# Performance work log

Measured on AMD Instinct MI355X. Metric: run time of the kernel, lower is better.

Reference implementation:

```python
import jax, jax.numpy as jnp
import numpy as np

B, L, E, V = 4, 2048, 1024, 64
NT = V * (V - 1) // 2  # 2016 upper-triangular entries
LN_EPS = 1e-5


def setup_inputs() -> dict:
    key = jax.random.key(0)
    ks = jax.random.split(key, 9)
    s = lambda d: 1.0 / np.sqrt(d)
    return {
        "hx": jax.random.normal(ks[0], (B, L, E), dtype=jnp.float32),
        "W_dense": jax.random.normal(ks[1], (E, E), dtype=jnp.float32) * s(E),
        "b_dense": jnp.zeros((E,), dtype=jnp.float32),
        "ln_g": jnp.ones((E,), dtype=jnp.float32),
        "ln_b": jnp.zeros((E,), dtype=jnp.float32),
        "W_theta": jax.random.normal(ks[2], (V, E), dtype=jnp.float32) * s(E),
        "b_theta": jnp.zeros((V,), dtype=jnp.float32),
        "W_Theta": jax.random.normal(ks[3], (NT, E), dtype=jnp.float32) * s(E),
        "b_Theta": jnp.zeros((NT,), dtype=jnp.float32),
    }


def reference(hx, W_dense, b_dense, ln_g, ln_b, W_theta, b_theta, W_Theta, b_Theta):
    # dense -> exact (erf) gelu -> LayerNorm (ESM1bLayerNorm)
    h = jax.nn.gelu(hx @ W_dense.T + b_dense, approximate=False)
    mu = jnp.mean(h, axis=-1, keepdims=True)
    var = jnp.mean(jnp.square(h - mu), axis=-1, keepdims=True)
    h = (h - mu) / jnp.sqrt(var + LN_EPS) * ln_g + ln_b

    pi = jax.nn.softmax(h @ W_theta.T + b_theta, axis=-1)          # (B,L,V)
    Theta = jax.nn.softplus(h @ W_Theta.T + b_Theta)               # (B,L,NT)

    iu, ju = np.triu_indices(V, k=1)
    S = jnp.zeros((B, L, V, V), dtype=h.dtype).at[:, :, iu, ju].set(Theta)
    S = S + jnp.swapaxes(S, -2, -1)                                # symmetric, zero diag

    # diag(1/sqrt(pi)) @ S @ diag(sqrt(pi)) == S * sqrt(pi_j)/sqrt(pi_i)
    pi_sqrt = jnp.sqrt(pi)
    Q = S * (pi_sqrt[..., None, :] / pi_sqrt[..., :, None])
    Q = Q - Q.sum(axis=-1)[..., :, None] * jnp.eye(V, dtype=Q.dtype)
    return (Q, pi)
```

## Files before the change

### kernel.cpp

```cpp
#include <hip/hip_runtime.h>
#include <hip/hip_bf16.h>
#include <cstdint>
#include <cstddef>

#define MROWS 8192
#define EDIM  1024
#define VDIM  64
#define NTRI  2016
#define NTC   2176

typedef _Float16 half8  __attribute__((ext_vector_type(8)));
typedef _Float16 half4v __attribute__((ext_vector_type(4)));
typedef float    floatx4 __attribute__((ext_vector_type(4)));

typedef __attribute__((address_space(1))) void gvoid;
typedef __attribute__((address_space(3))) void svoid;

__device__ inline void gld_lds16(const _Float16* g, _Float16* l) {
    __builtin_amdgcn_global_load_lds((gvoid*)g, (svoid*)l, 16, 0, 0);
}

__device__ inline float fast_erf(float x) {
    float ax = fabsf(x);
    float t = 1.0f / (1.0f + 0.3275911f * ax);
    float p = t * (0.254829592f +
              t * (-0.284496736f +
              t * (1.421413741f +
              t * (-1.453152027f +
              t * 1.061405429f))));
    float r = 1.0f - p * __expf(-ax * ax);
    return copysignf(r, x);
}

__device__ inline float fast_softplus(float x) {
    return fmaxf(x, 0.0f) + __logf(1.0f + __expf(-fabsf(x)));
}

__global__ __launch_bounds__(256) void cast_f2h(const float* __restrict__ in,
                                                _Float16* __restrict__ out,
                                                int n_valid, int n_total) {
    int idx = (blockIdx.x * 256 + threadIdx.x) * 4;
    if (idx >= n_total) return;
    half4v o;
    if (idx < n_valid) {
        float4 v = *(const float4*)(in + idx);
        o[0] = (_Float16)v.x; o[1] = (_Float16)v.y;
        o[2] = (_Float16)v.z; o[3] = (_Float16)v.w;
    } else {
        o[0] = (_Float16)0.f; o[1] = (_Float16)0.f;
        o[2] = (_Float16)0.f; o[3] = (_Float16)0.f;
    }
    *(half4v*)(out + idx) = o;
}

template <int MODE>
__global__ __launch_bounds__(256) void gemm_bt(const _Float16* __restrict__ A,
                                               const _Float16* __restrict__ Bt,
                                               const float* __restrict__ bias,
                                               const float* __restrict__ bias2,
                                               float* __restrict__ C, int N) {
    __shared__ __align__(16) _Float16 As[128 * 64];
    __shared__ __align__(16) _Float16 Bs[128 * 64];

    const int tid  = threadIdx.x;
    const int ng   = N >> 7;
    const int xcd  = blockIdx.x & 7;
    const int slot = blockIdx.x >> 3;
    const int mg   = slot / ng;
    const int nn   = slot - mg * ng;
    const int m0   = (xcd + mg * 8) * 128;
    const int n0   = nn * 128;

    const int w    = tid >> 6;
    const int lane = tid & 63;
    const int wr   = w >> 1;
    const int wc   = w & 1;
    const int lrow  = lane & 15;
    const int lquad = lane >> 4;

    floatx4 acc[4][4] = {};

    const int r0 = tid >> 3;
    const int c0 = tid & 7;
    const int g  = (c0 ^ (r0 & 7)) * 8;
    const _Float16* Ag[4];
    const _Float16* Bg[4];
#pragma unroll
    for (int call = 0; call < 4; ++call) {
        Ag[call] = A  + (size_t)(m0 + call * 32 + r0) * EDIM + g;
        Bg[call] = Bt + (size_t)(n0 + call * 32 + r0) * EDIM + g;
    }
    _Float16* AsD = &As[tid * 8];
    _Float16* BsD = &Bs[tid * 8];

    const int swr = lrow & 7;
    const _Float16* ardA = &As[(wr * 64 + lrow) * 64];
    const _Float16* brdB = &Bs[(wc * 64 + lrow) * 64];

    for (int k0 = 0; k0 < EDIM; k0 += 64) {
#pragma unroll
        for (int call = 0; call < 4; ++call) {
            gld_lds16(Ag[call] + k0, AsD + call * 2048);
            gld_lds16(Bg[call] + k0, BsD + call * 2048);
        }
        __syncthreads();

#pragma unroll
        for (int kstep = 0; kstep < 2; ++kstep) {
            const int soff = ((kstep * 4 + lquad) ^ swr) * 8;
            half8 af[4], bf[4];
#pragma unroll
            for (int t = 0; t < 4; ++t) {
                af[t] = *(const half8*)(ardA + t * 16 * 64 + soff);
                bf[t] = *(const half8*)(brdB + t * 16 * 64 + soff);
            }
#pragma unroll
            for (int i = 0; i < 4; ++i)
#pragma unroll
                for (int j = 0; j < 4; ++j)
                    acc[i][j] = __builtin_amdgcn_mfma_f32_16x16x32_f16(
                        af[i], bf[j], acc[i][j], 0, 0, 0);
        }
        __syncthreads();
    }

    const int cm = m0 + wr * 64 + lquad * 4;
    const int cn = n0 + wc * 64 + lrow;
#pragma unroll
    for (int j = 0; j < 4; ++j) {
        const int gn = cn + j * 16;
        float bv;
        if (MODE == 0) {
            bv = bias[gn];
        } else {
            if (gn < NTRI)             bv = bias[gn];
            else if (gn < NTRI + VDIM) bv = bias2[gn - NTRI];
            else                       bv = 0.0f;
        }
#pragma unroll
        for (int i = 0; i < 4; ++i) {
#pragma unroll
            for (int r = 0; r < 4; ++r) {
                float x = acc[i][j][r] + bv;
                float y;
                if (MODE == 0) {
                    y = 0.5f * x * (1.0f + fast_erf(x * 0.70710678118654752f));
                } else {
                    if (gn < NTRI) {
                        y = fast_softplus(x);
                    } else if (gn < NTRI + VDIM) {
                        y = x;
                    } else {
                        y = 0.0f;
                    }
                }
                C[(size_t)(cm + i * 16 + r) * N + gn] = y;
            }
        }
    }
}

__global__ __launch_bounds__(256) void ln_kernel(float* __restrict__ H,
                                                 const float* __restrict__ gw,
                                                 const float* __restrict__ bw,
                                                 _Float16* __restrict__ Hh) {
    const int row = blockIdx.x, tid = threadIdx.x;
    float4 v = ((const float4*)(H + (size_t)row * EDIM))[tid];
    float s  = v.x + v.y + v.z + v.w;
    float ss = v.x * v.x + v.y * v.y + v.z * v.z + v.w * v.w;
#pragma unroll
    for (int off = 32; off; off >>= 1) {
        s  += __shfl_down(s, off);
        ss += __shfl_down(ss, off);
    }
    __shared__ float red[8];
    const int w = tid >> 6, lane = tid & 63;
    if (lane == 0) { red[w] = s; red[4 + w] = ss; }
    __syncthreads();
    const float st  = red[0] + red[1] + red[2] + red[3];
    const float sst = red[4] + red[5] + red[6] + red[7];
    const float mu  = st * (1.0f / EDIM);
    const float rs  = 1.0f / sqrtf(sst * (1.0f / EDIM) - mu * mu + 1e-5f);
    float4 gg = ((const float4*)gw)[tid];
    float4 bb = ((const float4*)bw)[tid];
    float4 y;
    y.x = (v.x - mu) * rs * gg.x + bb.x;
    y.y = (v.y - mu) * rs * gg.y + bb.y;
    y.z = (v.z - mu) * rs * gg.z + bb.z;
    y.w = (v.w - mu) * rs * gg.w + bb.w;
    ((float4*)(H + (size_t)row * EDIM))[tid] = y;
    half4v h4;
    h4[0] = (_Float16)y.x; h4[1] = (_Float16)y.y;
    h4[2] = (_Float16)y.z; h4[3] = (_Float16)y.w;
    ((half4v*)(Hh + (size_t)row * EDIM))[tid] = h4;
}

__global__ __launch_bounds__(256) void softmax_kernel(const float* __restrict__ Theta,
                                                      float* __restrict__ pi_out,
                                                      float* __restrict__ sp) {
    const int lane = threadIdx.x & 63;
    const int row  = blockIdx.x * 4 + (threadIdx.x >> 6);
    float lg = Theta[(size_t)row * NTC + NTRI + lane];
    float m = lg;
#pragma unroll
    for (int off = 32; off; off >>= 1) m = fmaxf(m, __shfl_xor(m, off));
    float e = __expf(lg - m);
    float ssum = e;
#pragma unroll
    for (int off = 32; off; off >>= 1) ssum += __shfl_xor(ssum, off);
    float p = e / ssum;
    pi_out[(size_t)row * VDIM + lane] = p;
    sp[(size_t)row * VDIM + lane] = sqrtf(p);
}

__global__ __launch_bounds__(256) void q_kernel(const float* __restrict__ Theta,
                                                const float* __restrict__ sp,
                                                float* __restrict__ Q) {
    const int row = blockIdx.x;
    __shared__ float Th[NTRI];
    __shared__ float spv[VDIM];
    const float* trow = Theta + (size_t)row * NTC;
    for (int t = threadIdx.x; t < NTRI; t += 256) Th[t] = trow[t];
    if (threadIdx.x < VDIM) spv[threadIdx.x] = sp[(size_t)row * VDIM + threadIdx.x];
    __syncthreads();

    const int i = threadIdx.x >> 2;
    const int q = threadIdx.x & 3;
    const float rpi = 1.0f / spv[i];
    float vals[16];
    float psum = 0.f;
#pragma unroll
    for (int c = 0; c < 16; ++c) {
        const int j = q * 16 + c;
        float out = 0.f;
        if (j != i) {
            const int a = (i < j) ? i : j;
            const int b = (i < j) ? j : i;
            const int t = a * (127 - a) / 2 + (b - a - 1);
            out = Th[t] * spv[j] * rpi;
            psum += out;
        }
        vals[c] = out;
    }
    psum += __shfl_xor(psum, 1);
    psum += __shfl_xor(psum, 2);

    float* qrow = Q + ((size_t)row * VDIM + i) * VDIM + q * 16;
    float4* dst = (float4*)qrow;
    dst[0] = make_float4(vals[0], vals[1], vals[2], vals[3]);
    dst[1] = make_float4(vals[4], vals[5], vals[6], vals[7]);
    dst[2] = make_float4(vals[8], vals[9], vals[10], vals[11]);
    dst[3] = make_float4(vals[12], vals[13], vals[14], vals[15]);
    if ((i >> 4) == q) {
        Q[((size_t)row * VDIM + i) * VDIM + i] = -psum;
    }
}

extern "C" void kernel_launch(void* const* d_in, const int* in_sizes, int n_in,
                              void* d_out, int out_size, void* d_ws, size_t ws_size,
                              hipStream_t stream) {
    const float* hx      = (const float*)d_in[0];
    const float* W_dense = (const float*)d_in[1];
    const float* b_dense = (const float*)d_in[2];
    const float* ln_g    = (const float*)d_in[3];
    const float* ln_b    = (const float*)d_in[4];
    const float* W_theta = (const float*)d_in[5];
    const float* b_theta = (const float*)d_in[6];
    const float* W_Theta = (const float*)d_in[7];
    const float* b_Theta = (const float*)d_in[8];

    uint8_t* ws = (uint8_t*)d_ws;
    _Float16* A_h  = (_Float16*)ws;
    _Float16* Wd_h = (_Float16*)(ws + (size_t)16 * 1048576);
    _Float16* Wc_h = (_Float16*)(ws + (size_t)18 * 1048576);
    float*    G    = (float*)(ws + (size_t)23 * 1048576);
    float*    Theta= (float*)(ws + (size_t)23 * 1048576);
    float*    sp   = (float*)(ws + (size_t)92 * 1048576);

    float* Q_out  = (float*)d_out;
    float* pi_out = (float*)d_out + (size_t)MROWS * VDIM * VDIM;

    cast_f2h<<<(MROWS * EDIM / 4) / 256, 256, 0, stream>>>(hx, A_h, MROWS * EDIM, MROWS * EDIM);
    cast_f2h<<<(EDIM * EDIM / 4) / 256, 256, 0, stream>>>(W_dense, Wd_h, EDIM * EDIM, EDIM * EDIM);
    cast_f2h<<<(NTRI * EDIM / 4) / 256, 256, 0, stream>>>(W_Theta, Wc_h, NTRI * EDIM, NTRI * EDIM);
    cast_f2h<<<((NTC - NTRI) * EDIM / 4) / 256, 256, 0, stream>>>(
        W_theta, Wc_h + (size_t)NTRI * EDIM, VDIM * EDIM, (NTC - NTRI) * EDIM);

    gemm_bt<0><<<(EDIM / 128) * (MROWS / 128), 256, 0, stream>>>(
        A_h, Wd_h, b_dense, nullptr, G, EDIM);

    ln_kernel<<<MROWS, 256, 0, stream>>>(G, ln_g, ln_b, A_h);

    gemm_bt<1><<<(NTC / 128) * (MROWS / 128), 256, 0, stream>>>(
        A_h, Wc_h, b_Theta, b_theta, Theta, NTC);

    softmax_kernel<<<MROWS / 4, 256, 0, stream>>>(Theta, pi_out, sp);

    q_kernel<<<MROWS, 256, 0, stream>>>(Theta, sp, Q_out);
}
```

Baseline: 349.9 us.

## Store GEMM outputs in fp16, fuse softmax into Q kernel, drop LN fp32 writeback

Both GEMMs now write their intermediate outputs in fp16 instead of fp32, which halves the traffic for G and Theta. The LayerNorm kernel no longer writes back an fp32 copy of its output. The softmax kernel is merged into the Q kernel, so the sp buffer and one launch go away. The diagonal entry of Q is now written inside the vector stores instead of as a separate scalar store. In exchange, the logits and Theta values carry fp16 rounding, which costs some precision.

```diff
diff --git a/kernel.cpp b/kernel.cpp
--- a/kernel.cpp
+++ b/kernel.cpp
@@ -58,7 +58,7 @@
                                                const _Float16* __restrict__ Bt,
                                                const float* __restrict__ bias,
                                                const float* __restrict__ bias2,
-                                               float* __restrict__ C, int N) {
+                                               _Float16* __restrict__ C, int N) {
     __shared__ __align__(16) _Float16 As[128 * 64];
     __shared__ __align__(16) _Float16 Bs[128 * 64];
 
@@ -154,20 +154,21 @@
                         y = 0.0f;
                     }
                 }
-                C[(size_t)(cm + i * 16 + r) * N + gn] = y;
+                C[(size_t)(cm + i * 16 + r) * N + gn] = (_Float16)y;
             }
         }
     }
 }
 
-__global__ __launch_bounds__(256) void ln_kernel(float* __restrict__ H,
+__global__ __launch_bounds__(256) void ln_kernel(const _Float16* __restrict__ G,
                                                  const float* __restrict__ gw,
                                                  const float* __restrict__ bw,
                                                  _Float16* __restrict__ Hh) {
     const int row = blockIdx.x, tid = threadIdx.x;
-    float4 v = ((const float4*)(H + (size_t)row * EDIM))[tid];
-    float s  = v.x + v.y + v.z + v.w;
-    float ss = v.x * v.x + v.y * v.y + v.z * v.z + v.w * v.w;
+    half4v v = ((const half4v*)(G + (size_t)row * EDIM))[tid];
+    float x0 = (float)v[0], x1 = (float)v[1], x2 = (float)v[2], x3 = (float)v[3];
+    float s  = x0 + x1 + x2 + x3;
+    float ss = x0 * x0 + x1 * x1 + x2 * x2 + x3 * x3;
 #pragma unroll
     for (int off = 32; off; off >>= 1) {
         s  += __shfl_down(s, off);
@@ -183,49 +184,45 @@
     const float rs  = 1.0f / sqrtf(sst * (1.0f / EDIM) - mu * mu + 1e-5f);
     float4 gg = ((const float4*)gw)[tid];
     float4 bb = ((const float4*)bw)[tid];
-    float4 y;
-    y.x = (v.x - mu) * rs * gg.x + bb.x;
-    y.y = (v.y - mu) * rs * gg.y + bb.y;
-    y.z = (v.z - mu) * rs * gg.z + bb.z;
-    y.w = (v.w - mu) * rs * gg.w + bb.w;
-    ((float4*)(H + (size_t)row * EDIM))[tid] = y;
     half4v h4;
-    h4[0] = (_Float16)y.x; h4[1] = (_Float16)y.y;
-    h4[2] = (_Float16)y.z; h4[3] = (_Float16)y.w;
+    h4[0] = (_Float16)((x0 - mu) * rs * gg.x + bb.x);
+    h4[1] = (_Float16)((x1 - mu) * rs * gg.y + bb.y);
+    h4[2] = (_Float16)((x2 - mu) * rs * gg.z + bb.z);
+    h4[3] = (_Float16)((x3 - mu) * rs * gg.w + bb.w);
     ((half4v*)(Hh + (size_t)row * EDIM))[tid] = h4;
 }
 
-__global__ __launch_bounds__(256) void softmax_kernel(const float* __restrict__ Theta,
-                                                      float* __restrict__ pi_out,
-                                                      float* __restrict__ sp) {
-    const int lane = threadIdx.x & 63;
-    const int row  = blockIdx.x * 4 + (threadIdx.x >> 6);
-    float lg = Theta[(size_t)row * NTC + NTRI + lane];
-    float m = lg;
-#pragma unroll
-    for (int off = 32; off; off >>= 1) m = fmaxf(m, __shfl_xor(m, off));
-    float e = __expf(lg - m);
-    float ssum = e;
-#pragma unroll
-    for (int off = 32; off; off >>= 1) ssum += __shfl_xor(ssum, off);
-    float p = e / ssum;
-    pi_out[(size_t)row * VDIM + lane] = p;
-    sp[(size_t)row * VDIM + lane] = sqrtf(p);
-}
-
-__global__ __launch_bounds__(256) void q_kernel(const float* __restrict__ Theta,
-                                                const float* __restrict__ sp,
+__global__ __launch_bounds__(256) void q_kernel(const _Float16* __restrict__ Theta,
+                                                float* __restrict__ pi_out,
                                                 float* __restrict__ Q) {
     const int row = blockIdx.x;
+    const int tid = threadIdx.x;
     __shared__ float Th[NTRI];
     __shared__ float spv[VDIM];
-    const float* trow = Theta + (size_t)row * NTC;
-    for (int t = threadIdx.x; t < NTRI; t += 256) Th[t] = trow[t];
-    if (threadIdx.x < VDIM) spv[threadIdx.x] = sp[(size_t)row * VDIM + threadIdx.x];
+    const _Float16* trow = Theta + (size_t)row * NTC;
+    if (tid < 252) {
+        half8 h = *(const half8*)(trow + tid * 8);
+#pragma unroll
+        for (int u = 0; u < 8; ++u) Th[tid * 8 + u] = (float)h[u];
+    }
+    if (tid >= 192) {
+        const int lane = tid & 63;
+        float lg = (float)trow[NTRI + lane];
+        float m = lg;
+#pragma unroll
+        for (int off = 32; off; off >>= 1) m = fmaxf(m, __shfl_xor(m, off));
+        float e = __expf(lg - m);
+        float ssum = e;
+#pragma unroll
+        for (int off = 32; off; off >>= 1) ssum += __shfl_xor(ssum, off);
+        float p = e / ssum;
+        pi_out[(size_t)row * VDIM + lane] = p;
+        spv[lane] = sqrtf(p);
+    }
     __syncthreads();
 
-    const int i = threadIdx.x >> 2;
-    const int q = threadIdx.x & 3;
+    const int i = tid >> 2;
+    const int q = tid & 3;
     const float rpi = 1.0f / spv[i];
     float vals[16];
     float psum = 0.f;
@@ -244,6 +241,7 @@
     }
     psum += __shfl_xor(psum, 1);
     psum += __shfl_xor(psum, 2);
+    if ((i >> 4) == q) vals[i & 15] = -psum;
 
     float* qrow = Q + ((size_t)row * VDIM + i) * VDIM + q * 16;
     float4* dst = (float4*)qrow;
@@ -251,9 +249,6 @@
     dst[1] = make_float4(vals[4], vals[5], vals[6], vals[7]);
     dst[2] = make_float4(vals[8], vals[9], vals[10], vals[11]);
     dst[3] = make_float4(vals[12], vals[13], vals[14], vals[15]);
-    if ((i >> 4) == q) {
-        Q[((size_t)row * VDIM + i) * VDIM + i] = -psum;
-    }
 }
 
 extern "C" void kernel_launch(void* const* d_in, const int* in_sizes, int n_in,
@@ -273,9 +268,8 @@
     _Float16* A_h  = (_Float16*)ws;
     _Float16* Wd_h = (_Float16*)(ws + (size_t)16 * 1048576);
     _Float16* Wc_h = (_Float16*)(ws + (size_t)18 * 1048576);
-    float*    G    = (float*)(ws + (size_t)23 * 1048576);
-    float*    Theta= (float*)(ws + (size_t)23 * 1048576);
-    float*    sp   = (float*)(ws + (size_t)92 * 1048576);
+    _Float16* G_h  = (_Float16*)(ws + (size_t)23 * 1048576);
+    _Float16* Th_h = (_Float16*)(ws + (size_t)23 * 1048576);
 
     float* Q_out  = (float*)d_out;
     float* pi_out = (float*)d_out + (size_t)MROWS * VDIM * VDIM;
@@ -287,14 +281,12 @@
         W_theta, Wc_h + (size_t)NTRI * EDIM, VDIM * EDIM, (NTC - NTRI) * EDIM);
 
     gemm_bt<0><<<(EDIM / 128) * (MROWS / 128), 256, 0, stream>>>(
-        A_h, Wd_h, b_dense, nullptr, G, EDIM);
-
-    ln_kernel<<<MROWS, 256, 0, stream>>>(G, ln_g, ln_b, A_h);
+        A_h, Wd_h, b_dense, nullptr, G_h, EDIM);
+
+    ln_kernel<<<MROWS, 256, 0, stream>>>(G_h, ln_g, ln_b, A_h);
 
     gemm_bt<1><<<(NTC / 128) * (MROWS / 128), 256, 0, stream>>>(
-        A_h, Wc_h, b_Theta, b_theta, Theta, NTC);
-
-    softmax_kernel<<<MROWS / 4, 256, 0, stream>>>(Theta, pi_out, sp);
-
-    q_kernel<<<MROWS, 256, 0, stream>>>(Theta, sp, Q_out);
-}
+        A_h, Wc_h, b_Theta, b_theta, Th_h, NTC);
+
+    q_kernel<<<MROWS, 256, 0, stream>>>(Th_h, pi_out, Q_out);
+}
```

New measurement: 320.4 us. 1.09x faster.
